# Kernel optimization log

Measured on AMD Instinct MI355X. Metric: run time of the kernel, lower is better.

## Reference

```python
import math
import jax, jax.numpy as jnp
import numpy as np

B, S, E, H = 2, 2048, 1024, 16
Dh = E // H  # 64
ROPE_BASE = 10000.0


def setup_inputs() -> dict:
    key = jax.random.key(0)
    ks = jax.random.split(key, 7)
    f32 = jnp.float32
    return {
        "q": jax.random.normal(ks[0], (B, S, E), dtype=f32),
        "k": jax.random.normal(ks[1], (B, S, E), dtype=f32),
        "v": jax.random.normal(ks[2], (B, S, E), dtype=f32),
        # nn.Linear weights stored torch-style as [out_features, in_features]
        "W_q": jax.random.normal(ks[3], (E, E), dtype=f32) * 0.02,
        "W_k": jax.random.normal(ks[4], (E, E), dtype=f32) * 0.02,
        "W_v": jax.random.normal(ks[5], (E, E), dtype=f32) * 0.02,
        "W_o": jax.random.normal(ks[6], (E, E), dtype=f32) * 0.02,
    }


def _rope(x):
    # x: [B, H, S, Dh]; interleaved-pair rotary embedding along the seq axis.
    d = x.shape[-1]
    pos = jnp.arange(x.shape[2], dtype=x.dtype)
    inv_freq = 1.0 / (ROPE_BASE ** (jnp.arange(0, d, 2, dtype=x.dtype) / d))
    ang = pos[:, None] * inv_freq            # [S, Dh//2]
    cos, sin = jnp.cos(ang), jnp.sin(ang)    # broadcast over [B, H]
    xe, xo = x[..., 0::2], x[..., 1::2]      # even/odd interleaved pairs
    out = jnp.stack([xe * cos - xo * sin, xo * cos + xe * sin], axis=-1)
    return out.reshape(x.shape)


def reference(q, k, v, W_q, W_k, W_v, W_o):
    b, s, e = q.shape
    scale = 1.0 / math.sqrt(e)  # NOTE: 1/sqrt(hidden_dim), not head_dim (faithful)
    # project and split heads: [B, H, S, Dh]
    qh = (q @ W_q.T).reshape(b, s, H, Dh).transpose(0, 2, 1, 3)
    kh = (k @ W_k.T).reshape(b, s, H, Dh).transpose(0, 2, 1, 3)
    vh = (v @ W_v.T).reshape(b, s, H, Dh).transpose(0, 2, 1, 3)
    qh = _rope(qh)
    kh = _rope(kh)
    scores = jnp.einsum('bhsd,bhtd->bhst', qh, kh) * scale
    # Faithful quirk: the original sets causal_mask[0,0] = False, which zeroes
    # the ENTIRE [S,S] mask (dims 0,1 are singletons) -> masked_fill is a no-op.
    probs = jax.nn.softmax(scores, axis=-1)
    out = jnp.einsum('bhst,bhtd->bhsd', probs, vh)
    out = out.transpose(0, 2, 1, 3).reshape(b, s, e)
    return out @ W_o.T
```

## Files before the change

kernel.cpp:

```cpp
#include <hip/hip_runtime.h>
#include <math.h>

#define Bsz 2
#define Ssz 2048
#define Esz 1024
#define Hn  16
#define Dd  64
#define PADC 72
#define TP   136
#define FP   68

typedef unsigned short ushort_t;
typedef short bf16x8 __attribute__((ext_vector_type(8)));
typedef short bf16x4 __attribute__((ext_vector_type(4)));
typedef float f32x4 __attribute__((ext_vector_type(4)));

#define GLD16(g, l) __builtin_amdgcn_global_load_lds(                        \
    (const __attribute__((address_space(1))) unsigned int*)(g),              \
    (__attribute__((address_space(3))) unsigned int*)(l), 16, 0, 0)

#define KF 0.045084220027780106f

#define MFMA32(a, b, c) __builtin_amdgcn_mfma_f32_16x16x32_bf16((a), (b), (c), 0, 0, 0)
#define MFMA16(a, b, c) __builtin_amdgcn_mfma_f32_16x16x16bf16_1k((a), (b), (c), 0, 0, 0)

__device__ inline ushort_t bf16_rn(float x)
{
    unsigned u = __float_as_uint(x);
    return (ushort_t)((u + 0x7FFFu + ((u >> 16) & 1u)) >> 16);
}

__global__ __launch_bounds__(256) void cvt_kernel(
    const float* s0, const float* s1, const float* s2, const float* s3,
    const float* s4, const float* s5, const float* s6,
    ushort_t* d0, ushort_t* d1, ushort_t* d2, ushort_t* d3,
    ushort_t* d4, ushort_t* d5, ushort_t* d6,
    float* tc, float* ts, int n_big, int n_small)
{
    if (blockIdx.z == 7) {
        const int idx = blockIdx.x * 256 + threadIdx.x;
        if (idx < Ssz * 32) {
            const int s = idx >> 5, p = idx & 31;
            const double c = 9.210340371976184257 / 32.0;
            const double inv = exp(-c * (double)p);
            double sn, cs;
            sincos((double)s * inv, &sn, &cs);
            tc[idx] = (float)cs;
            ts[idx] = (float)sn;
        }
        return;
    }
    const float* s; ushort_t* d;
    switch (blockIdx.z) {
        case 0: s = s0; d = d0; break;
        case 1: s = s1; d = d1; break;
        case 2: s = s2; d = d2; break;
        case 3: s = s3; d = d3; break;
        case 4: s = s4; d = d4; break;
        case 5: s = s5; d = d5; break;
        default: s = s6; d = d6; break;
    }
    const int n = (blockIdx.z < 3) ? n_big : n_small;
    const int i = (blockIdx.x * 256 + threadIdx.x) * 4;
    if (i >= n) return;
    float4 v = *(const float4*)(s + i);
    ushort4 o;
    o.x = bf16_rn(v.x); o.y = bf16_rn(v.y);
    o.z = bf16_rn(v.z); o.w = bf16_rn(v.w);
    *(ushort4*)(d + i) = o;
}

__global__ __launch_bounds__(256) void proj_gemm_kernel(
    const ushort_t* __restrict__ Aq, const ushort_t* __restrict__ Ak,
    const ushort_t* __restrict__ Av,
    const ushort_t* __restrict__ Wq, const ushort_t* __restrict__ Wk,
    const ushort_t* __restrict__ Wv,
    ushort_t* __restrict__ Yq, ushort_t* __restrict__ Yk,
    ushort_t* __restrict__ Yv,
    const float* __restrict__ tc, const float* __restrict__ ts)
{
    const int z = blockIdx.z;
    const ushort_t* Ag = (z == 0) ? Aq : (z == 1) ? Ak : Av;
    const ushort_t* Wg = (z == 0) ? Wq : (z == 1) ? Wk : Wv;
    ushort_t*       Yg = (z == 0) ? Yq : (z == 1) ? Yk : Yv;

    __shared__ __align__(16) ushort_t sA[128 * 32];
    __shared__ __align__(16) ushort_t sB[128 * 32];
    __shared__ __align__(16) ushort_t Tb[128 * TP];

    const int t    = threadIdx.x;
    const int lane = t & 63;
    const int w    = t >> 6;
    const int wm   = (w & 1) * 64;
    const int wn   = (w >> 1) * 64;
    const int fr   = lane & 15;
    const int g    = lane >> 4;
    const int kq   = g * 8;
    const int n0   = blockIdx.x * 128;
    const int m0   = blockIdx.y * 128;

    const ushort_t* pA = Ag + (size_t)(m0 + (t >> 2)) * 1024 + (t & 3) * 8;
    const ushort_t* pB = Wg + (size_t)(n0 + (t >> 2)) * 1024 + (t & 3) * 8;

    f32x4 acc[4][4];
#pragma unroll
    for (int mi = 0; mi < 4; ++mi)
#pragma unroll
        for (int ni = 0; ni < 4; ++ni) acc[mi][ni] = (f32x4)0.f;

    for (int k0 = 0; k0 < 1024; k0 += 32) {
        GLD16(pA + k0,             &sA[t * 8]);
        GLD16(pA + k0 + 64 * 1024, &sA[2048 + t * 8]);
        GLD16(pB + k0,             &sB[t * 8]);
        GLD16(pB + k0 + 64 * 1024, &sB[2048 + t * 8]);
        __syncthreads();

        bf16x8 a[4], b[4];
#pragma unroll
        for (int mi = 0; mi < 4; ++mi)
            a[mi] = *(const bf16x8*)&sA[(wm + mi * 16 + fr) * 32 + kq];
#pragma unroll
        for (int ni = 0; ni < 4; ++ni)
            b[ni] = *(const bf16x8*)&sB[(wn + ni * 16 + fr) * 32 + kq];
#pragma unroll
        for (int mi = 0; mi < 4; ++mi)
#pragma unroll
            for (int ni = 0; ni < 4; ++ni)
                acc[mi][ni] = MFMA32(a[mi], b[ni], acc[mi][ni]);
        __syncthreads();
    }

#pragma unroll
    for (int mi = 0; mi < 4; ++mi)
#pragma unroll
        for (int ni = 0; ni < 4; ++ni) {
            const int col = wn + ni * 16 + fr;
            const int d   = (n0 + col) & 63;
            const int pi  = d >> 1;
#pragma unroll
            for (int rg = 0; rg < 4; ++rg) {
                const int row = wm + mi * 16 + g * 4 + rg;
                const int s   = (m0 + row) & (Ssz - 1);
                float v  = acc[mi][ni][rg];
                float pt = __shfl_xor(v, 1, 64);
                float o  = v;
                if (z < 2) {
                    const float cs = tc[s * 32 + pi];
                    const float sn = ts[s * 32 + pi];
                    o = (d & 1) ? fmaf(v, cs, pt * sn)
                                : fmaf(v, cs, -pt * sn);
                    if (z == 0) o *= KF;
                }
                Tb[row * TP + col] = bf16_rn(o);
            }
        }
    __syncthreads();

    if (z < 2) {
        const int row = t >> 1;
        const int m   = m0 + row;
        const int b   = m >> 11, s = m & (Ssz - 1);
#pragma unroll
        for (int i = 0; i < 8; ++i) {
            const int ic = (t & 1) * 8 + i;
            uint4 val = *(const uint4*)&Tb[row * TP + ic * 8];
            const int hh = (n0 >> 6) + (ic >> 3);
            const int d  = (ic & 7) * 8;
            *(uint4*)&Yg[(((size_t)(b * Hn + hh)) * Ssz + s) * Dd + d] = val;
        }
    } else {
        const int col = t >> 1;
        const int hh  = (n0 >> 6) + (col >> 6);
        const int d   = col & 63;
        const int b   = m0 >> 11;
        const int sg  = (m0 & (Ssz - 1)) + (t & 1) * 64;
        const size_t base = (((size_t)(b * Hn + hh)) * Dd + d) * Ssz + sg;
#pragma unroll
        for (int jj = 0; jj < 8; ++jj) {
            uint4 val;
            unsigned vv[4];
#pragma unroll
            for (int qd = 0; qd < 4; ++qd) {
                const int r0 = (t & 1) * 64 + jj * 8 + qd * 2;
                const unsigned lo = Tb[(r0 + 0) * TP + col];
                const unsigned hi = Tb[(r0 + 1) * TP + col];
                vv[qd] = lo | (hi << 16);
            }
            val.x = vv[0]; val.y = vv[1]; val.z = vv[2]; val.w = vv[3];
            *(uint4*)&Yg[base + jj * 8] = val;
        }
    }
}

__global__ __launch_bounds__(256) void attn_kernel(
    const ushort_t* __restrict__ Qb, const ushort_t* __restrict__ Kb,
    const ushort_t* __restrict__ Vtb, ushort_t* __restrict__ Ob)
{
    __shared__ __align__(16) ushort_t sK[64 * PADC];
    __shared__ __align__(16) ushort_t sV[64 * PADC];

    const int t    = threadIdx.x;
    const int lane = t & 63;
    const int w    = t >> 6;
    const int fr   = lane & 15;
    const int g    = lane >> 4;
    const int kq   = g * 8;
    const int bh   = blockIdx.y;
    const int q0   = blockIdx.x * 128;

    bf16x8 qa[2][2];
#pragma unroll
    for (int mt = 0; mt < 2; ++mt) {
        const size_t qbase = ((size_t)bh * Ssz + q0 + w * 32 + mt * 16 + fr) * Dd;
        qa[mt][0] = *(const bf16x8*)(Qb + qbase + kq);
        qa[mt][1] = *(const bf16x8*)(Qb + qbase + 32 + kq);
    }

    float lp[2] = {0.f, 0.f};
    f32x4 Oacc[2][4];
#pragma unroll
    for (int mt = 0; mt < 2; ++mt)
#pragma unroll
        for (int dt = 0; dt < 4; ++dt) Oacc[mt][dt] = (f32x4)0.f;

    const int srow = t >> 3;
    const int scol = (t & 7) * 8;
    const size_t kgb = (size_t)bh * Ssz * Dd;
    const size_t vgb = (size_t)bh * Dd * Ssz;

    for (int kv0 = 0; kv0 < Ssz; kv0 += 64) {
#pragma unroll
        for (int rr = 0; rr < 2; ++rr) {
            const int row = srow + rr * 32;
            *(uint4*)&sK[row * PADC + scol] =
                *(const uint4*)(Kb + kgb + (size_t)(kv0 + row) * Dd + scol);
            *(uint4*)&sV[row * PADC + scol] =
                *(const uint4*)(Vtb + vgb + (size_t)row * Ssz + kv0 + scol);
        }
        __syncthreads();

        f32x4 St[2][4];
#pragma unroll
        for (int mt = 0; mt < 2; ++mt)
#pragma unroll
            for (int nt = 0; nt < 4; ++nt) St[mt][nt] = (f32x4)0.f;
#pragma unroll
        for (int ks = 0; ks < 2; ++ks)
#pragma unroll
            for (int nt = 0; nt < 4; ++nt) {
                bf16x8 kfrag = *(const bf16x8*)&sK[(nt * 16 + fr) * PADC + ks * 32 + kq];
#pragma unroll
                for (int mt = 0; mt < 2; ++mt)
                    St[mt][nt] = MFMA32(kfrag, qa[mt][ks], St[mt][nt]);
            }

        bf16x4 pf[2][4];
#pragma unroll
        for (int mt = 0; mt < 2; ++mt)
#pragma unroll
            for (int nt = 0; nt < 4; ++nt) {
                const float p0 = exp2f(St[mt][nt][0]);
                const float p1 = exp2f(St[mt][nt][1]);
                const float p2 = exp2f(St[mt][nt][2]);
                const float p3 = exp2f(St[mt][nt][3]);
                lp[mt] += (p0 + p1) + (p2 + p3);
                union { unsigned u[2]; bf16x4 s; } pk;
                pk.u[0] = (__float_as_uint(p0) >> 16) | (__float_as_uint(p1) & 0xFFFF0000u);
                pk.u[1] = (__float_as_uint(p2) >> 16) | (__float_as_uint(p3) & 0xFFFF0000u);
                pf[mt][nt] = pk.s;
            }

#pragma unroll
        for (int nt = 0; nt < 4; ++nt)
#pragma unroll
            for (int dt = 0; dt < 4; ++dt) {
                bf16x4 vfrag = *(const bf16x4*)&sV[(dt * 16 + fr) * PADC + nt * 16 + g * 4];
#pragma unroll
                for (int mt = 0; mt < 2; ++mt)
                    Oacc[mt][dt] = MFMA16(pf[mt][nt], vfrag, Oacc[mt][dt]);
            }
        __syncthreads();
    }

#pragma unroll
    for (int mt = 0; mt < 2; ++mt) {
        lp[mt] += __shfl_xor(lp[mt], 16, 64);
        lp[mt] += __shfl_xor(lp[mt], 32, 64);
    }

    const int b = bh >> 4, h = bh & 15;
#pragma unroll
    for (int mt = 0; mt < 2; ++mt)
#pragma unroll
        for (int rg = 0; rg < 4; ++rg) {
            const float lv  = __shfl(lp[mt], (lane & 48) + g * 4 + rg, 64);
            const float inv = 1.f / lv;
            const int s = q0 + w * 32 + mt * 16 + g * 4 + rg;
#pragma unroll
            for (int dt = 0; dt < 4; ++dt) {
                const float o = Oacc[mt][dt][rg] * inv;
                Ob[((size_t)(b * Ssz + s)) * Esz + h * Dd + dt * 16 + fr] = bf16_rn(o);
            }
        }
}

__global__ __launch_bounds__(256) void final_gemm_kernel(
    const ushort_t* __restrict__ Ag, const ushort_t* __restrict__ Bg,
    float* __restrict__ Yf)
{
    __shared__ __align__(16) ushort_t sA[128 * 32];
    __shared__ __align__(16) ushort_t sB[128 * 32];
    __shared__ __align__(16) float Tf[128 * FP];

    const int t    = threadIdx.x;
    const int lane = t & 63;
    const int w    = t >> 6;
    const int wm   = (w & 1) * 64;
    const int wn   = (w >> 1) * 64;
    const int fr   = lane & 15;
    const int g    = lane >> 4;
    const int kq   = g * 8;
    const int n0   = blockIdx.x * 128;
    const int m0   = blockIdx.y * 128;

    const ushort_t* pA = Ag + (size_t)(m0 + (t >> 2)) * 1024 + (t & 3) * 8;
    const ushort_t* pB = Bg + (size_t)(n0 + (t >> 2)) * 1024 + (t & 3) * 8;

    f32x4 acc[4][4];
#pragma unroll
    for (int mi = 0; mi < 4; ++mi)
#pragma unroll
        for (int ni = 0; ni < 4; ++ni) acc[mi][ni] = (f32x4)0.f;

    for (int k0 = 0; k0 < 1024; k0 += 32) {
        GLD16(pA + k0,             &sA[t * 8]);
        GLD16(pA + k0 + 64 * 1024, &sA[2048 + t * 8]);
        GLD16(pB + k0,             &sB[t * 8]);
        GLD16(pB + k0 + 64 * 1024, &sB[2048 + t * 8]);
        __syncthreads();

        bf16x8 a[4], b[4];
#pragma unroll
        for (int mi = 0; mi < 4; ++mi)
            a[mi] = *(const bf16x8*)&sA[(wm + mi * 16 + fr) * 32 + kq];
#pragma unroll
        for (int ni = 0; ni < 4; ++ni)
            b[ni] = *(const bf16x8*)&sB[(wn + ni * 16 + fr) * 32 + kq];
#pragma unroll
        for (int mi = 0; mi < 4; ++mi)
#pragma unroll
            for (int ni = 0; ni < 4; ++ni)
                acc[mi][ni] = MFMA32(a[mi], b[ni], acc[mi][ni]);
        __syncthreads();
    }

#pragma unroll
    for (int hf = 0; hf < 2; ++hf) {
        if ((w >> 1) == hf) {
#pragma unroll
            for (int mi = 0; mi < 4; ++mi)
#pragma unroll
                for (int ni = 0; ni < 4; ++ni) {
                    const int col = ni * 16 + fr;
#pragma unroll
                    for (int rg = 0; rg < 4; ++rg)
                        Tf[(wm + mi * 16 + g * 4 + rg) * FP + col] = acc[mi][ni][rg];
                }
        }
        __syncthreads();
        const int row = t >> 1;
        float* dst = Yf + (size_t)(m0 + row) * 1024 + n0 + hf * 64 + (t & 1) * 32;
        const float* src = &Tf[row * FP + (t & 1) * 32];
#pragma unroll
        for (int i = 0; i < 8; ++i)
            *(float4*)(dst + i * 4) = *(const float4*)(src + i * 4);
        __syncthreads();
    }
}

extern "C" void kernel_launch(void* const* d_in, const int* in_sizes, int n_in,
                              void* d_out, int out_size, void* d_ws, size_t ws_size,
                              hipStream_t stream)
{
    (void)in_sizes; (void)n_in; (void)out_size; (void)ws_size;
    const float* q   = (const float*)d_in[0];
    const float* k   = (const float*)d_in[1];
    const float* v   = (const float*)d_in[2];
    const float* W_q = (const float*)d_in[3];
    const float* W_k = (const float*)d_in[4];
    const float* W_v = (const float*)d_in[5];
    const float* W_o = (const float*)d_in[6];
    float* out = (float*)d_out;

    const size_t NQ = (size_t)Bsz * Ssz * Esz;
    const size_t NW = (size_t)Esz * Esz;

    float* ws = (float*)d_ws;
    float* tc = ws;
    float* ts = ws + 65536;

    ushort_t* us  = (ushort_t*)(ws + 131072);
    ushort_t* qb  = us;
    ushort_t* kb  = qb + NQ;
    ushort_t* vb  = kb + NQ;
    ushort_t* wqb = vb + NQ;
    ushort_t* wkb = wqb + NW;
    ushort_t* wvb = wkb + NW;
    ushort_t* wob = wvb + NW;
    ushort_t* pq  = wob + NW;
    ushort_t* pk  = pq + NQ;
    ushort_t* pv  = pk + NQ;
    ushort_t* ob  = pv + NQ;

    dim3 blk(256);

    cvt_kernel<<<dim3(4096, 1, 8), blk, 0, stream>>>(
        q, k, v, W_q, W_k, W_v, W_o,
        qb, kb, vb, wqb, wkb, wvb, wob, tc, ts, (int)NQ, (int)NW);

    proj_gemm_kernel<<<dim3(Esz / 128, (Bsz * Ssz) / 128, 3), blk, 0, stream>>>(
        qb, kb, vb, wqb, wkb, wvb, pq, pk, pv, tc, ts);

    attn_kernel<<<dim3(Ssz / 128, Bsz * Hn), blk, 0, stream>>>(pq, pk, pv, ob);

    final_gemm_kernel<<<dim3(Esz / 128, (Bsz * Ssz) / 128), blk, 0, stream>>>(
        ob, wob, out);
}
```

Measured before the change: 295.9 us.

## Double-buffer attention K/V tiles, alias GEMM smem, shrink output GEMM tile

The attention kernel now prefetches the next K/V tile into registers while computing on the current one. It writes that tile into a second shared-memory buffer, which cuts one barrier per iteration and hides global load latency. The projection and output GEMMs alias their staging and epilogue shared memory so each block uses less LDS and more blocks can be resident. The output GEMM drops to 128x64 tiles with twice as many blocks, raising occupancy on a small grid at the cost of re-reading A twice as often and more register pressure from the prefetch in attention.

```diff
diff --git a/kernel.cpp b/kernel.cpp
--- a/kernel.cpp
+++ b/kernel.cpp
@@ -84,9 +84,10 @@
     const ushort_t* Wg = (z == 0) ? Wq : (z == 1) ? Wk : Wv;
     ushort_t*       Yg = (z == 0) ? Yq : (z == 1) ? Yk : Yv;
 
-    __shared__ __align__(16) ushort_t sA[128 * 32];
-    __shared__ __align__(16) ushort_t sB[128 * 32];
-    __shared__ __align__(16) ushort_t Tb[128 * TP];
+    __shared__ __align__(16) char smem[128 * TP * 2];
+    ushort_t* sA = (ushort_t*)smem;
+    ushort_t* sB = sA + 128 * 32;
+    ushort_t* Tb = (ushort_t*)smem;
 
     const int t    = threadIdx.x;
     const int lane = t & 63;
@@ -196,8 +197,7 @@
     const ushort_t* __restrict__ Qb, const ushort_t* __restrict__ Kb,
     const ushort_t* __restrict__ Vtb, ushort_t* __restrict__ Ob)
 {
-    __shared__ __align__(16) ushort_t sK[64 * PADC];
-    __shared__ __align__(16) ushort_t sV[64 * PADC];
+    __shared__ __align__(16) ushort_t sKV[4][64 * PADC];
 
     const int t    = threadIdx.x;
     const int lane = t & 63;
@@ -228,16 +228,30 @@
     const size_t kgb = (size_t)bh * Ssz * Dd;
     const size_t vgb = (size_t)bh * Dd * Ssz;
 
+#pragma unroll
+    for (int rr = 0; rr < 2; ++rr) {
+        const int row = srow + rr * 32;
+        *(uint4*)&sKV[0][row * PADC + scol] =
+            *(const uint4*)(Kb + kgb + (size_t)row * Dd + scol);
+        *(uint4*)&sKV[2][row * PADC + scol] =
+            *(const uint4*)(Vtb + vgb + (size_t)row * Ssz + scol);
+    }
+    __syncthreads();
+
+    int cur = 0;
     for (int kv0 = 0; kv0 < Ssz; kv0 += 64) {
-#pragma unroll
-        for (int rr = 0; rr < 2; ++rr) {
-            const int row = srow + rr * 32;
-            *(uint4*)&sK[row * PADC + scol] =
-                *(const uint4*)(Kb + kgb + (size_t)(kv0 + row) * Dd + scol);
-            *(uint4*)&sV[row * PADC + scol] =
-                *(const uint4*)(Vtb + vgb + (size_t)row * Ssz + kv0 + scol);
-        }
-        __syncthreads();
+        const bool more = (kv0 + 64 < Ssz);
+        uint4 nk[2], nv[2];
+        if (more) {
+#pragma unroll
+            for (int rr = 0; rr < 2; ++rr) {
+                const int row = srow + rr * 32;
+                nk[rr] = *(const uint4*)(Kb + kgb + (size_t)(kv0 + 64 + row) * Dd + scol);
+                nv[rr] = *(const uint4*)(Vtb + vgb + (size_t)row * Ssz + kv0 + 64 + scol);
+            }
+        }
+        const ushort_t* sK = sKV[cur];
+        const ushort_t* sV = sKV[2 + cur];
 
         f32x4 St[2][4];
 #pragma unroll
@@ -279,7 +293,17 @@
                 for (int mt = 0; mt < 2; ++mt)
                     Oacc[mt][dt] = MFMA16(pf[mt][nt], vfrag, Oacc[mt][dt]);
             }
-        __syncthreads();
+
+        if (more) {
+#pragma unroll
+            for (int rr = 0; rr < 2; ++rr) {
+                const int row = srow + rr * 32;
+                *(uint4*)&sKV[cur ^ 1][row * PADC + scol] = nk[rr];
+                *(uint4*)&sKV[2 + (cur ^ 1)][row * PADC + scol] = nv[rr];
+            }
+            __syncthreads();
+            cur ^= 1;
+        }
     }
 
 #pragma unroll
@@ -308,74 +332,69 @@
     const ushort_t* __restrict__ Ag, const ushort_t* __restrict__ Bg,
     float* __restrict__ Yf)
 {
-    __shared__ __align__(16) ushort_t sA[128 * 32];
-    __shared__ __align__(16) ushort_t sB[128 * 32];
-    __shared__ __align__(16) float Tf[128 * FP];
+    __shared__ __align__(16) char smem[128 * FP * 4];
+    ushort_t* sA = (ushort_t*)smem;
+    ushort_t* sB = sA + 128 * 32;
+    float*    Tf = (float*)smem;
 
     const int t    = threadIdx.x;
     const int lane = t & 63;
     const int w    = t >> 6;
     const int wm   = (w & 1) * 64;
-    const int wn   = (w >> 1) * 64;
+    const int wn   = (w >> 1) * 32;
     const int fr   = lane & 15;
     const int g    = lane >> 4;
     const int kq   = g * 8;
-    const int n0   = blockIdx.x * 128;
+    const int n0   = blockIdx.x * 64;
     const int m0   = blockIdx.y * 128;
 
     const ushort_t* pA = Ag + (size_t)(m0 + (t >> 2)) * 1024 + (t & 3) * 8;
     const ushort_t* pB = Bg + (size_t)(n0 + (t >> 2)) * 1024 + (t & 3) * 8;
 
-    f32x4 acc[4][4];
+    f32x4 acc[4][2];
 #pragma unroll
     for (int mi = 0; mi < 4; ++mi)
 #pragma unroll
-        for (int ni = 0; ni < 4; ++ni) acc[mi][ni] = (f32x4)0.f;
+        for (int ni = 0; ni < 2; ++ni) acc[mi][ni] = (f32x4)0.f;
 
     for (int k0 = 0; k0 < 1024; k0 += 32) {
         GLD16(pA + k0,             &sA[t * 8]);
         GLD16(pA + k0 + 64 * 1024, &sA[2048 + t * 8]);
         GLD16(pB + k0,             &sB[t * 8]);
-        GLD16(pB + k0 + 64 * 1024, &sB[2048 + t * 8]);
         __syncthreads();
 
-        bf16x8 a[4], b[4];
+        bf16x8 a[4], b[2];
 #pragma unroll
         for (int mi = 0; mi < 4; ++mi)
             a[mi] = *(const bf16x8*)&sA[(wm + mi * 16 + fr) * 32 + kq];
 #pragma unroll
-        for (int ni = 0; ni < 4; ++ni)
+        for (int ni = 0; ni < 2; ++ni)
             b[ni] = *(const bf16x8*)&sB[(wn + ni * 16 + fr) * 32 + kq];
 #pragma unroll
         for (int mi = 0; mi < 4; ++mi)
 #pragma unroll
-            for (int ni = 0; ni < 4; ++ni)
+            for (int ni = 0; ni < 2; ++ni)
                 acc[mi][ni] = MFMA32(a[mi], b[ni], acc[mi][ni]);
         __syncthreads();
     }
 
 #pragma unroll
-    for (int hf = 0; hf < 2; ++hf) {
-        if ((w >> 1) == hf) {
-#pragma unroll
-            for (int mi = 0; mi < 4; ++mi)
-#pragma unroll
-                for (int ni = 0; ni < 4; ++ni) {
-                    const int col = ni * 16 + fr;
-#pragma unroll
-                    for (int rg = 0; rg < 4; ++rg)
-                        Tf[(wm + mi * 16 + g * 4 + rg) * FP + col] = acc[mi][ni][rg];
-                }
-        }
-        __syncthreads();
-        const int row = t >> 1;
-        float* dst = Yf + (size_t)(m0 + row) * 1024 + n0 + hf * 64 + (t & 1) * 32;
-        const float* src = &Tf[row * FP + (t & 1) * 32];
-#pragma unroll
-        for (int i = 0; i < 8; ++i)
-            *(float4*)(dst + i * 4) = *(const float4*)(src + i * 4);
-        __syncthreads();
-    }
+    for (int mi = 0; mi < 4; ++mi)
+#pragma unroll
+        for (int ni = 0; ni < 2; ++ni) {
+            const int col = wn + ni * 16 + fr;
+#pragma unroll
+            for (int rg = 0; rg < 4; ++rg)
+                Tf[(wm + mi * 16 + g * 4 + rg) * FP + col] = acc[mi][ni][rg];
+        }
+    __syncthreads();
+
+    const int row = t >> 1;
+    float* dst = Yf + (size_t)(m0 + row) * 1024 + n0 + (t & 1) * 32;
+    const float* src = &Tf[row * FP + (t & 1) * 32];
+#pragma unroll
+    for (int i = 0; i < 8; ++i)
+        *(float4*)(dst + i * 4) = *(const float4*)(src + i * 4);
 }
 
 extern "C" void kernel_launch(void* const* d_in, const int* in_sizes, int n_in,
@@ -423,6 +442,6 @@
 
     attn_kernel<<<dim3(Ssz / 128, Bsz * Hn), blk, 0, stream>>>(pq, pk, pv, ob);
 
-    final_gemm_kernel<<<dim3(Esz / 128, (Bsz * Ssz) / 128), blk, 0, stream>>>(
+    final_gemm_kernel<<<dim3(Esz / 64, (Bsz * Ssz) / 128), blk, 0, stream>>>(
         ob, wob, out);
 }
```

New measurement: 302.0 us. 1.02x slower.
